# Kernel optimization log

Measured on AMD Instinct MI355X. Metric: run time of the kernel, lower is better.

Reference implementation:

```python
import jax, jax.numpy as jnp
import numpy as np

N_HEAD = 16
D_HEAD = 64
D_MODEL = 1024  # d_qry = d_key = d_val
D_HIDDEN = N_HEAD * D_HEAD


def setup_inputs() -> dict:
    key = jax.random.key(0)
    ks = jax.random.split(key, 9)
    b, n = 2, 2048
    s = 0.02
    return {
        "qry": jax.random.normal(ks[0], (b, n, D_MODEL), jnp.float32),
        "key": jax.random.normal(ks[1], (b, n, D_MODEL), jnp.float32),
        "val": jax.random.normal(ks[2], (b, n, D_MODEL), jnp.float32),
        "mask": jax.random.randint(ks[3], (b, n), 0, 2) > 0,  # key-side padding mask
        "Wq": jax.random.normal(ks[4], (D_MODEL, D_HIDDEN), jnp.float32) * s,
        "Wk": jax.random.normal(ks[5], (D_MODEL, D_HIDDEN), jnp.float32) * s,
        "Wv": jax.random.normal(ks[6], (D_MODEL, D_HIDDEN), jnp.float32) * s,
        "Wo": jax.random.normal(ks[7], (D_HIDDEN, D_MODEL), jnp.float32) * s,
        "bo": jax.random.normal(ks[8], (D_MODEL,), jnp.float32) * s,
    }


def reference(qry, key, val, mask, Wq, Wk, Wv, Wo, bo):
    b, n, _ = qry.shape
    scale = D_HEAD ** 0.5
    # projections, split into heads: [b, h, n, d]
    q = (qry @ Wq).reshape(b, n, N_HEAD, D_HEAD).transpose(0, 2, 1, 3)
    k = (key @ Wk).reshape(b, n, N_HEAD, D_HEAD).transpose(0, 2, 1, 3)
    v = (val @ Wv).reshape(b, n, N_HEAD, D_HEAD).transpose(0, 2, 1, 3)
    sim = jnp.einsum('bhid,bhjd->bhij', q, k) / scale  # full O(n^2) scores
    # key-side padding mask broadcast over heads and query positions
    sim = jnp.where(mask[:, None, None, :], sim, jnp.float32(-1e32))
    attn = jax.nn.softmax(sim, axis=-1)
    # NOTE: original applies dropout to `sim` after computing attn (a no-op on
    # the output); dropout=0.0 regardless, so attention weights are `attn`.
    x = jnp.einsum('bhij,bhjd->bhid', attn, v)
    x = x.transpose(0, 2, 1, 3).reshape(b, n, D_HIDDEN)
    return x @ Wo + bo
```

## Files before the change

kernel.cpp:

```cpp
#include <hip/hip_runtime.h>
#include <hip/hip_bf16.h>

using u16 = unsigned short;
using u32 = unsigned int;
using short8 = __attribute__((ext_vector_type(8))) short;
using f32x4  = __attribute__((ext_vector_type(4))) float;
using u32x4  = __attribute__((ext_vector_type(4))) u32;
using u32x2  = __attribute__((ext_vector_type(2))) u32;

union V16 { u32x4 u; short8 s; };

__device__ __forceinline__ u16 f2b(float f) {
  u32 u = __float_as_uint(f);
  u32 r = (u + 0x7FFFu + ((u >> 16) & 1u)) >> 16;
  return (u16)r;
}
__device__ __forceinline__ u32 pk2(u16 a, u16 b) {
  return (u32)a | ((u32)b << 16);
}
__device__ __forceinline__ u32 cvtpk(float lo, float hi) {
  u32 r;
  asm("v_cvt_pk_bf16_f32 %0, %1, %2" : "=v"(r) : "v"(lo), "v"(hi));
  return r;
}
__device__ __forceinline__ float ex2(float x) {
  float r;
  asm("v_exp_f32 %0, %1" : "=v"(r) : "v"(x));
  return r;
}
__device__ __forceinline__ void gld16(const u16* g, u16* l) {
  __builtin_amdgcn_global_load_lds(
      (const __attribute__((address_space(1))) u32*)g,
      (__attribute__((address_space(3))) u32*)l, 16, 0, 0);
}

#define KSCALE 0.18033688011f
#define SMAX   12.0f


__global__ __launch_bounds__(256) void wconv(
    const float* __restrict__ Wq, const float* __restrict__ Wk,
    const float* __restrict__ Wv, const float* __restrict__ Wo,
    u16* __restrict__ Wt, u16* __restrict__ WoT)
{
  __shared__ u16 T[64][130];
  const int zz = blockIdx.z;
  const float* src = (zz == 0) ? Wq : (zz == 1) ? Wk : (zz == 2) ? Wv : Wo;
  u16* dst = (zz < 3) ? (Wt + (size_t)zz * 1048576) : WoT;
  const int nt = blockIdx.x, ks = blockIdx.y;
  const int tid = threadIdx.x;

  {
    const int kl = tid >> 2, nl0 = (tid & 3) * 32;
    const float* sp = src + (size_t)(ks * 64 + kl) * 1024 + nt * 128 + nl0;
#pragma unroll
    for (int i = 0; i < 8; ++i) {
      f32x4 x = *(const f32x4*)(sp + i * 4);
      T[kl][nl0 + i * 4 + 0] = f2b(x[0]);
      T[kl][nl0 + i * 4 + 1] = f2b(x[1]);
      T[kl][nl0 + i * 4 + 2] = f2b(x[2]);
      T[kl][nl0 + i * 4 + 3] = f2b(x[3]);
    }
  }
  __syncthreads();

  const int c = tid >> 4, l0 = (tid & 15) * 4;
  u16* dp = dst + ((size_t)(nt * 16 + ks) * 16 + c) * 512 + l0 * 8;
#pragma unroll
  for (int dl = 0; dl < 4; ++dl) {
    const int l = l0 + dl;
    const int kl = (c & 1) * 32 + (l >> 4) * 8;
    const int nl = (c >> 3) * 64 + ((c >> 1) & 3) * 16 + (l & 15);
    u32x4 u;
#pragma unroll
    for (int p = 0; p < 4; ++p)
      u[p] = pk2(T[kl + 2 * p][nl], T[kl + 2 * p + 1][nl]);
    *(u32x4*)(dp + dl * 8) = u;
  }
}

__global__ __launch_bounds__(256) void aconv(
    const float* __restrict__ Aq, const float* __restrict__ Ak,
    const float* __restrict__ Av, u16* __restrict__ Af,
    int z0, size_t zstride)
{
  const int z = blockIdx.z + z0;
  const float* A = (z == 0) ? Aq : (z == 1) ? Ak : Av;
  u16* dst = Af + (size_t)blockIdx.z * zstride;
  const int ks = blockIdx.x, mt = blockIdx.y;
  const int tid = threadIdx.x;
  const int r = tid >> 1, h = tid & 1;

  const f32x4* sp = (const f32x4*)(A + (size_t)(mt * 128 + r) * 1024 + ks * 64 + h * 32);
  const int c = ((r >> 6) << 3) | (((r >> 4) & 3) << 1) | h;
  u16* dp = dst + ((size_t)(mt * 16 + ks) * 16 + c) * 512 + (r & 15) * 8;

#pragma unroll
  for (int lg = 0; lg < 4; ++lg) {
    f32x4 x0 = sp[2 * lg], x1 = sp[2 * lg + 1];
    u32x4 u;
    u[0] = cvtpk(x0[0], x0[1]); u[1] = cvtpk(x0[2], x0[3]);
    u[2] = cvtpk(x1[0], x1[1]); u[3] = cvtpk(x1[2], x1[3]);
    *(u32x4*)(dp + lg * 128) = u;
  }
}

__global__ __launch_bounds__(256) void maskscan(
    const int* __restrict__ mask, int* __restrict__ cidx,
    float* __restrict__ cbias, int* __restrict__ ntb,
    u16* __restrict__ Kimg, u16* __restrict__ Vimg)
{
  const int h = blockIdx.x, b = blockIdx.y;
  const int tid = threadIdx.x;
  __shared__ int ssum[256];

  int m8[8], s = 0;
#pragma unroll
  for (int i = 0; i < 8; ++i) {
    m8[i] = mask[b * 2048 + tid * 8 + i] ? 1 : 0;
    s += m8[i];
  }
  ssum[tid] = s;
  __syncthreads();
  for (int off = 1; off < 256; off <<= 1) {
    int v = (tid >= off) ? ssum[tid - off] : 0;
    __syncthreads();
    ssum[tid] += v;
    __syncthreads();
  }
  const int nvalid = ssum[255];
  int run = ssum[tid] - s;

  if (h == 0) {
#pragma unroll
    for (int i = 0; i < 8; ++i) {
      cidx[b * 2048 + tid * 8 + i] = m8[i] ? run : -1;
      run += m8[i];
    }
#pragma unroll
    for (int i = 0; i < 8; ++i) {
      const int idx = tid * 8 + i;
      cbias[b * 2048 + idx] = (idx < nvalid) ? -SMAX : -1e30f;
    }
    if (tid == 0) ntb[b] = (nvalid + 63) >> 6;
  }

  const int pend = ((nvalid + 63) >> 6) << 6;
  for (int p = nvalid + tid; p < pend; p += 256) {
    const int kt2 = p >> 6, r = p & 63;
    const size_t base = ((size_t)((b * 16 + h) * 32 + kt2)) * 4096;
    const int t2 = ((r >> 5) << 1) | ((r >> 2) & 1);
    const int ll2 = (((r >> 3) & 3) << 2) | (r & 3);
#pragma unroll
    for (int s2 = 0; s2 < 2; ++s2)
#pragma unroll
      for (int lgk = 0; lgk < 4; ++lgk)
#pragma unroll
        for (int e = 0; e < 8; ++e)
          Kimg[base + (t2 * 2 + s2) * 512 + (lgk * 16 + ll2) * 8 + e] = 0;
    const int sv = r >> 5, lgv = (r >> 3) & 3, e0 = r & 7;
#pragma unroll
    for (int td = 0; td < 4; ++td)
#pragma unroll
      for (int llv = 0; llv < 16; ++llv)
        Vimg[base + (sv * 4 + td) * 512 + (lgv * 16 + llv) * 8 + e0] = 0;
  }
}

__global__ __launch_bounds__(512, 4) void gemm_qkv_k(
    const u16* __restrict__ Af, const u16* __restrict__ Wt,
    u16* __restrict__ Qw, u16* __restrict__ Kw, u16* __restrict__ Vw,
    const int* __restrict__ cidx, int z0, size_t azs)
{
  __shared__ u16 As[2][8192];
  __shared__ u16 Bs[2][8192];

  const int L = blockIdx.x;
  const int xcd = L & 7, idx = L >> 3;
  const int mt = (xcd << 2) | (idx & 3);
  const int nt = (idx >> 2) & 7;
  const int zi = idx >> 5;
  const int z = z0 + zi;

  const u16* Aimg = Af + (size_t)zi * azs;
  const u16* Bimg = Wt + (size_t)z * 1048576;
  u16* O = (z == 0) ? Qw : (z == 1) ? Kw : Vw;

  const int tid = threadIdx.x;
  const int w = tid >> 6, l = tid & 63, lg = l >> 4, ll = l & 15;
  const int wr = w >> 2, wc = w & 3;
  const size_t ab = (size_t)mt * 131072;
  const size_t bb = (size_t)nt * 131072;

  f32x4 acc[4][2];
#pragma unroll
  for (int i = 0; i < 4; ++i)
#pragma unroll
    for (int t = 0; t < 2; ++t)
      acc[i][t] = (f32x4){0.f, 0.f, 0.f, 0.f};

#define QKV_ISSUE(ksx, buf) do {                                           \
    const size_t ao_ = ab + (size_t)(ksx) * 8192;                          \
    const size_t bo_ = bb + (size_t)(ksx) * 8192;                          \
    gld16(Aimg + ao_ + (size_t)w * 512 + l * 8,       &As[buf][w * 512]);  \
    gld16(Aimg + ao_ + (size_t)(w + 8) * 512 + l * 8, &As[buf][(w + 8) * 512]); \
    gld16(Bimg + bo_ + (size_t)w * 512 + l * 8,       &Bs[buf][w * 512]);  \
    gld16(Bimg + bo_ + (size_t)(w + 8) * 512 + l * 8, &Bs[buf][(w + 8) * 512]); \
  } while (0)

  QKV_ISSUE(0, 0);

  for (int ks = 0; ks < 16; ++ks) {
    const int cur = ks & 1;
    asm volatile("s_waitcnt vmcnt(0)" ::: "memory");
    __builtin_amdgcn_sched_barrier(0);
    __builtin_amdgcn_s_barrier();
    __builtin_amdgcn_sched_barrier(0);

    if (ks + 1 < 16) QKV_ISSUE(ks + 1, cur ^ 1);

    short8 afr[2][4], bfr[2][2];
#pragma unroll
    for (int kk = 0; kk < 2; ++kk) {
#pragma unroll
      for (int i = 0; i < 4; ++i) {
        V16 v; v.u = *(const u32x4*)&As[cur][(wr * 8 + i * 2 + kk) * 512 + l * 8];
        afr[kk][i] = v.s;
      }
#pragma unroll
      for (int t = 0; t < 2; ++t) {
        V16 v; v.u = *(const u32x4*)&Bs[cur][((wc >> 1) * 8 + ((wc & 1) * 2 + t) * 2 + kk) * 512 + l * 8];
        bfr[kk][t] = v.s;
      }
    }
#pragma unroll
    for (int kk = 0; kk < 2; ++kk)
#pragma unroll
      for (int i = 0; i < 4; ++i)
#pragma unroll
        for (int t = 0; t < 2; ++t)
          acc[i][t] = __builtin_amdgcn_mfma_f32_16x16x32_bf16(afr[kk][i], bfr[kk][t], acc[i][t], 0, 0, 0);
  }
#undef QKV_ISSUE

  const int m0 = mt * 128, n0 = nt * 128;
  if (z == 0) {
#pragma unroll
    for (int i = 0; i < 4; ++i)
#pragma unroll
      for (int t = 0; t < 2; ++t) {
        const int n = n0 + wc * 32 + t * 16 + ll;
        const int h = n >> 6, dd = n & 63;
#pragma unroll
        for (int j = 0; j < 4; ++j) {
          const int m = m0 + wr * 64 + i * 16 + lg * 4 + j;
          const int bbk = m >> 11, pos = m & 2047;
          O[((size_t)(bbk * 16 + h) * 2048 + pos) * 64 + dd] = f2b(acc[i][t][j]);
        }
      }
  } else if (z == 1) {
#pragma unroll
    for (int i = 0; i < 4; ++i)
#pragma unroll
      for (int t = 0; t < 2; ++t) {
        const int n = n0 + wc * 32 + t * 16 + ll;
        const int h = n >> 6, dd = n & 63;
        const int s = dd >> 5, lgk = (dd >> 3) & 3, e = dd & 7;
        const int m_ = m0 + wr * 64 + i * 16 + lg * 4;
        const int bbk = m_ >> 11, pos0 = m_ & 2047;
        const int4 cp = *(const int4*)&cidx[bbk * 2048 + pos0];
        const int cpa[4] = {cp.x, cp.y, cp.z, cp.w};
#pragma unroll
        for (int j = 0; j < 4; ++j) {
          const int pp = cpa[j];
          if (pp >= 0) {
            const int kt2 = pp >> 6, r = pp & 63;
            const int t2 = ((r >> 5) << 1) | ((r >> 2) & 1);
            const int ll2 = (((r >> 3) & 3) << 2) | (r & 3);
            O[((size_t)((bbk * 16 + h) * 32 + kt2)) * 4096 + (t2 * 2 + s) * 512 + (lgk * 16 + ll2) * 8 + e]
                = f2b(acc[i][t][j] * KSCALE);
          }
        }
      }
  } else {
#pragma unroll
    for (int i = 0; i < 4; ++i)
#pragma unroll
      for (int t = 0; t < 2; ++t) {
        const int n = n0 + wc * 32 + t * 16 + ll;
        const int h = n >> 6, dd = n & 63;
        const int td = dd >> 4, llv = dd & 15;
        const int m_ = m0 + wr * 64 + i * 16 + lg * 4;
        const int bbk = m_ >> 11, pos0 = m_ & 2047;
        const int4 cp = *(const int4*)&cidx[bbk * 2048 + pos0];
        const int cpa[4] = {cp.x, cp.y, cp.z, cp.w};
#pragma unroll
        for (int j = 0; j < 4; ++j) {
          const int pp = cpa[j];
          if (pp >= 0) {
            const int kt2 = pp >> 6, kk = pp & 63;
            const int s = kk >> 5, lgv = (kk >> 3) & 3, e0 = kk & 7;
            O[((size_t)((bbk * 16 + h) * 32 + kt2)) * 4096 + (s * 4 + td) * 512 + (lgv * 16 + llv) * 8 + e0]
                = f2b(acc[i][t][j]);
          }
        }
      }
  }
}

__global__ __launch_bounds__(256) void attn_k(
    const u16* __restrict__ Q, const u16* __restrict__ Kt, const u16* __restrict__ Vt,
    const float* __restrict__ cbias, const int* __restrict__ ntb,
    u16* __restrict__ Xf)
{
  __shared__ u16 Ls[2][8192];

  const int tid = threadIdx.x;
  const int w = tid >> 6, l = tid & 63, lg = l >> 4, ll = l & 15;
  const int qb = blockIdx.x, h = blockIdx.y, b = blockIdx.z;
  const size_t qbase = (size_t)(b * 16 + h) * 2048 * 64;
  const size_t tbase = (size_t)((b * 16 + h) * 32) * 4096;
  const int q0 = qb * 128 + w * 32;
  const int ntiles = ntb[b];

  short8 aq[2][2];
#pragma unroll
  for (int g = 0; g < 2; ++g)
#pragma unroll
    for (int s = 0; s < 2; ++s) {
      V16 v; v.u = *(const u32x4*)&Q[qbase + (size_t)(q0 + g * 16 + ll) * 64 + s * 32 + lg * 8];
      aq[g][s] = v.s;
    }

  float lrow[2] = {0.f, 0.f};
  f32x4 o[2][4];
#pragma unroll
  for (int g = 0; g < 2; ++g)
#pragma unroll
    for (int td = 0; td < 4; ++td) o[g][td] = (f32x4){0.f, 0.f, 0.f, 0.f};

  u32x4 rg[4];
#pragma unroll
  for (int q = 0; q < 4; ++q) {
    const int c = w * 4 + q;
    const u16* src = (c < 8) ? Kt : Vt;
    rg[q] = *(const u32x4*)&src[tbase + (c & 7) * 512 + l * 8];
  }
#pragma unroll
  for (int q = 0; q < 4; ++q)
    *(u32x4*)&Ls[0][(w * 4 + q) * 512 + l * 8] = rg[q];
  if (ntiles > 1) {
#pragma unroll
    for (int q = 0; q < 4; ++q) {
      const int c = w * 4 + q;
      const u16* src = (c < 8) ? Kt : Vt;
      rg[q] = *(const u32x4*)&src[tbase + 4096 + (c & 7) * 512 + l * 8];
    }
  }
  asm volatile("s_waitcnt lgkmcnt(0)" ::: "memory");
  __builtin_amdgcn_sched_barrier(0);
  __builtin_amdgcn_s_barrier();
  __builtin_amdgcn_sched_barrier(0);

  for (int kt = 0; kt < ntiles; ++kt) {
    const int cur = kt & 1;
    const int j0 = kt * 64;
    const u16* Lc = Ls[cur];

    f32x4 sc[2][4];
    __builtin_amdgcn_s_setprio(1);
#pragma unroll
    for (int t = 0; t < 4; ++t) {
      short8 bk0, bk1;
      { V16 v; v.u = *(const u32x4*)&Lc[(t * 2 + 0) * 512 + l * 8]; bk0 = v.s; }
      { V16 v; v.u = *(const u32x4*)&Lc[(t * 2 + 1) * 512 + l * 8]; bk1 = v.s; }
      f32x4 a0 = (f32x4){0.f, 0.f, 0.f, 0.f};
      f32x4 a1 = (f32x4){0.f, 0.f, 0.f, 0.f};
      a0 = __builtin_amdgcn_mfma_f32_16x16x32_bf16(bk0, aq[0][0], a0, 0, 0, 0);
      a1 = __builtin_amdgcn_mfma_f32_16x16x32_bf16(bk0, aq[1][0], a1, 0, 0, 0);
      a0 = __builtin_amdgcn_mfma_f32_16x16x32_bf16(bk1, aq[0][1], a0, 0, 0, 0);
      a1 = __builtin_amdgcn_mfma_f32_16x16x32_bf16(bk1, aq[1][1], a1, 0, 0, 0);
      const f32x4 cb = *(const f32x4*)&cbias[b * 2048 + j0 + ((t >> 1) << 5) + ((t & 1) << 2) + (lg << 3)];
#pragma unroll
      for (int j = 0; j < 4; ++j) {
        sc[0][t][j] = a0[j] + cb[j];
        sc[1][t][j] = a1[j] + cb[j];
      }
    }
    __builtin_amdgcn_s_setprio(0);

#pragma unroll
    for (int g = 0; g < 2; ++g) {
      f32x4 s4 = (f32x4){0.f, 0.f, 0.f, 0.f};
#pragma unroll
      for (int t = 0; t < 4; ++t)
#pragma unroll
        for (int j = 0; j < 4; ++j) {
          sc[g][t][j] = ex2(sc[g][t][j]);
          s4[j] += sc[g][t][j];
        }
      float rs = (s4[0] + s4[1]) + (s4[2] + s4[3]);
      rs += __shfl_xor(rs, 16);
      rs += __shfl_xor(rs, 32);
      lrow[g] += rs;
    }

    __builtin_amdgcn_s_setprio(1);
#pragma unroll
    for (int s = 0; s < 2; ++s) {
      V16 pb0, pb1;
      pb0.u[0] = cvtpk(sc[0][2 * s][0], sc[0][2 * s][1]);
      pb0.u[1] = cvtpk(sc[0][2 * s][2], sc[0][2 * s][3]);
      pb0.u[2] = cvtpk(sc[0][2 * s + 1][0], sc[0][2 * s + 1][1]);
      pb0.u[3] = cvtpk(sc[0][2 * s + 1][2], sc[0][2 * s + 1][3]);
      pb1.u[0] = cvtpk(sc[1][2 * s][0], sc[1][2 * s][1]);
      pb1.u[1] = cvtpk(sc[1][2 * s][2], sc[1][2 * s][3]);
      pb1.u[2] = cvtpk(sc[1][2 * s + 1][0], sc[1][2 * s + 1][1]);
      pb1.u[3] = cvtpk(sc[1][2 * s + 1][2], sc[1][2 * s + 1][3]);
#pragma unroll
      for (int td = 0; td < 4; ++td) {
        V16 v; v.u = *(const u32x4*)&Lc[4096 + (s * 4 + td) * 512 + l * 8];
        o[0][td] = __builtin_amdgcn_mfma_f32_16x16x32_bf16(v.s, pb0.s, o[0][td], 0, 0, 0);
        o[1][td] = __builtin_amdgcn_mfma_f32_16x16x32_bf16(v.s, pb1.s, o[1][td], 0, 0, 0);
      }
    }
    __builtin_amdgcn_s_setprio(0);

    if (kt + 1 < ntiles) {
#pragma unroll
      for (int q = 0; q < 4; ++q)
        *(u32x4*)&Ls[cur ^ 1][(w * 4 + q) * 512 + l * 8] = rg[q];
    }
    if (kt + 2 < ntiles) {
#pragma unroll
      for (int q = 0; q < 4; ++q) {
        const int c = w * 4 + q;
        const u16* src = (c < 8) ? Kt : Vt;
        rg[q] = *(const u32x4*)&src[tbase + (size_t)(kt + 2) * 4096 + (c & 7) * 512 + l * 8];
      }
    }
    asm volatile("s_waitcnt lgkmcnt(0)" ::: "memory");
    __builtin_amdgcn_sched_barrier(0);
    __builtin_amdgcn_s_barrier();
    __builtin_amdgcn_sched_barrier(0);
  }

#pragma unroll
  for (int g = 0; g < 2; ++g) {
    const float inv = 1.f / lrow[g];
    const int m = b * 2048 + q0 + g * 16 + ll;
    const int mt = m >> 7, mr = m & 127;
    const int e0 = (lg & 1) * 4;
#pragma unroll
    for (int td = 0; td < 4; ++td) {
      const int c = ((mr >> 6) << 3) | (((mr >> 4) & 3) << 1) | (td >> 1);
      const int lA = (((td << 1) + (lg >> 1)) & 3) * 16 + (mr & 15);
      u32x2 wv;
      wv[0] = cvtpk(o[g][td][0] * inv, o[g][td][1] * inv);
      wv[1] = cvtpk(o[g][td][2] * inv, o[g][td][3] * inv);
      *(u32x2*)&Xf[((size_t)(mt * 16 + h) * 16 + c) * 512 + lA * 8 + e0] = wv;
    }
  }
}

__global__ __launch_bounds__(512, 4) void gemm_out_k(
    const u16* __restrict__ Xf, const u16* __restrict__ WoF,
    const float* __restrict__ bo, float* __restrict__ out)
{
  __shared__ u16 As[2][8192];
  __shared__ u16 Bs[2][8192];

  const int L = blockIdx.x;
  const int xcd = L & 7, idx = L >> 3;
  const int mt = (xcd << 2) | (idx & 3);
  const int nt = idx >> 2;

  const int tid = threadIdx.x;
  const int w = tid >> 6, l = tid & 63, lg = l >> 4, ll = l & 15;
  const int wr = w >> 2, wc = w & 3;
  const size_t ab = (size_t)mt * 131072;
  const size_t bb = (size_t)nt * 131072;

  f32x4 acc[4][2];
#pragma unroll
  for (int i = 0; i < 4; ++i)
#pragma unroll
    for (int t = 0; t < 2; ++t)
      acc[i][t] = (f32x4){0.f, 0.f, 0.f, 0.f};

#define OUT_ISSUE(ksx, buf) do {                                           \
    const size_t ao_ = ab + (size_t)(ksx) * 8192;                          \
    const size_t bo_ = bb + (size_t)(ksx) * 8192;                          \
    gld16(Xf + ao_ + (size_t)w * 512 + l * 8,        &As[buf][w * 512]);   \
    gld16(Xf + ao_ + (size_t)(w + 8) * 512 + l * 8,  &As[buf][(w + 8) * 512]); \
    gld16(WoF + bo_ + (size_t)w * 512 + l * 8,       &Bs[buf][w * 512]);   \
    gld16(WoF + bo_ + (size_t)(w + 8) * 512 + l * 8, &Bs[buf][(w + 8) * 512]); \
  } while (0)

  OUT_ISSUE(0, 0);

  for (int ks = 0; ks < 16; ++ks) {
    const int cur = ks & 1;
    asm volatile("s_waitcnt vmcnt(0)" ::: "memory");
    __builtin_amdgcn_sched_barrier(0);
    __builtin_amdgcn_s_barrier();
    __builtin_amdgcn_sched_barrier(0);

    if (ks + 1 < 16) OUT_ISSUE(ks + 1, cur ^ 1);

    short8 afr[2][4], bfr[2][2];
#pragma unroll
    for (int kk = 0; kk < 2; ++kk) {
#pragma unroll
      for (int i = 0; i < 4; ++i) {
        V16 v; v.u = *(const u32x4*)&As[cur][(wr * 8 + i * 2 + kk) * 512 + l * 8];
        afr[kk][i] = v.s;
      }
#pragma unroll
      for (int t = 0; t < 2; ++t) {
        V16 v; v.u = *(const u32x4*)&Bs[cur][((wc >> 1) * 8 + ((wc & 1) * 2 + t) * 2 + kk) * 512 + l * 8];
        bfr[kk][t] = v.s;
      }
    }
#pragma unroll
    for (int kk = 0; kk < 2; ++kk)
#pragma unroll
      for (int i = 0; i < 4; ++i)
#pragma unroll
        for (int t = 0; t < 2; ++t)
          acc[i][t] = __builtin_amdgcn_mfma_f32_16x16x32_bf16(afr[kk][i], bfr[kk][t], acc[i][t], 0, 0, 0);
  }
#undef OUT_ISSUE

  const int m0 = mt * 128, n0 = nt * 128;
#pragma unroll
  for (int i = 0; i < 4; ++i)
#pragma unroll
    for (int t = 0; t < 2; ++t) {
      const int n = n0 + wc * 32 + t * 16 + ll;
      const float bv = bo[n];
#pragma unroll
      for (int j = 0; j < 4; ++j) {
        const int m = m0 + wr * 64 + i * 16 + lg * 4 + j;
        out[(size_t)m * 1024 + n] = acc[i][t][j] + bv;
      }
    }
}

extern "C" void kernel_launch(void* const* d_in, const int* in_sizes, int n_in,
                              void* d_out, int out_size, void* d_ws, size_t ws_size,
                              hipStream_t stream) {
  const float* qry = (const float*)d_in[0];
  const float* key = (const float*)d_in[1];
  const float* val = (const float*)d_in[2];
  const int* mask  = (const int*)d_in[3];
  const float* Wq  = (const float*)d_in[4];
  const float* Wk  = (const float*)d_in[5];
  const float* Wv  = (const float*)d_in[6];
  const float* Wo  = (const float*)d_in[7];
  const float* bo  = (const float*)d_in[8];
  float* out = (float*)d_out;

  char* ws = (char*)d_ws;
  u16* Wt  = (u16*)(ws);
  u16* WoT = (u16*)(ws + 6291456);
  u16* Qw  = (u16*)(ws + 8388608);
  u16* Kw  = (u16*)(ws + 16777216);
  u16* Vw  = (u16*)(ws + 25165824);
  u16* Af  = (u16*)(ws + 33554432);
  u16* Xw  = (u16*)(ws + 33554432);

  int*   cidx  = (int*)d_out;
  float* cbias = (float*)((char*)d_out + 16384);
  int*   ntb   = (int*)((char*)d_out + 32768);

  wconv<<<dim3(8, 16, 4), 256, 0, stream>>>(Wq, Wk, Wv, Wo, Wt, WoT);
  maskscan<<<dim3(16, 2), 256, 0, stream>>>(mask, cidx, cbias, ntb, Kw, Vw);

  const bool big = (ws_size >= 58720256ull);
  if (big) {
    aconv<<<dim3(16, 32, 3), 256, 0, stream>>>(qry, key, val, Af, 0, 4194304);
    gemm_qkv_k<<<dim3(768, 1, 1), 512, 0, stream>>>(Af, Wt, Qw, Kw, Vw, cidx, 0, 4194304);
  } else {
    for (int z = 0; z < 3; ++z) {
      aconv<<<dim3(16, 32, 1), 256, 0, stream>>>(qry, key, val, Af, z, 0);
      gemm_qkv_k<<<dim3(256, 1, 1), 512, 0, stream>>>(Af, Wt, Qw, Kw, Vw, cidx, z, 0);
    }
  }
  attn_k<<<dim3(16, 16, 2), 256, 0, stream>>>(Qw, Kw, Vw, cbias, ntb, Xw);
  gemm_out_k<<<dim3(256, 1, 1), 512, 0, stream>>>(Xw, WoT, bo, out);
}
```

Measured before the change: 112.5 us.

## Widen QKV GEMM tile to 128x256 with triple-buffered half-K stages

```diff
diff --git a/kernel.cpp b/kernel.cpp
--- a/kernel.cpp
+++ b/kernel.cpp
@@ -172,84 +172,93 @@
     u16* __restrict__ Qw, u16* __restrict__ Kw, u16* __restrict__ Vw,
     const int* __restrict__ cidx, int z0, size_t azs)
 {
-  __shared__ u16 As[2][8192];
-  __shared__ u16 Bs[2][8192];
+  __shared__ u16 As[3][4096];
+  __shared__ u16 Bs[3][8192];
 
   const int L = blockIdx.x;
   const int xcd = L & 7, idx = L >> 3;
-  const int mt = (xcd << 2) | (idx & 3);
-  const int nt = (idx >> 2) & 7;
-  const int zi = idx >> 5;
-  const int z = z0 + zi;
+  const int mt  = (xcd << 2) | (idx & 3);
+  const int ntB = (idx >> 2) & 3;
+  const int zi  = idx >> 4;
+  const int z   = z0 + zi;
 
   const u16* Aimg = Af + (size_t)zi * azs;
-  const u16* Bimg = Wt + (size_t)z * 1048576;
+  const u16* B0 = Wt + (size_t)z * 1048576 + (size_t)(2 * ntB) * 131072;
+  const u16* B1 = B0 + 131072;
   u16* O = (z == 0) ? Qw : (z == 1) ? Kw : Vw;
 
   const int tid = threadIdx.x;
   const int w = tid >> 6, l = tid & 63, lg = l >> 4, ll = l & 15;
   const int wr = w >> 2, wc = w & 3;
-  const size_t ab = (size_t)mt * 131072;
-  const size_t bb = (size_t)nt * 131072;
-
-  f32x4 acc[4][2];
+  const size_t abase = (size_t)mt * 131072;
+
+  f32x4 acc[4][4];
 #pragma unroll
   for (int i = 0; i < 4; ++i)
 #pragma unroll
-    for (int t = 0; t < 2; ++t)
+    for (int t = 0; t < 4; ++t)
       acc[i][t] = (f32x4){0.f, 0.f, 0.f, 0.f};
 
-#define QKV_ISSUE(ksx, buf) do {                                           \
-    const size_t ao_ = ab + (size_t)(ksx) * 8192;                          \
-    const size_t bo_ = bb + (size_t)(ksx) * 8192;                          \
-    gld16(Aimg + ao_ + (size_t)w * 512 + l * 8,       &As[buf][w * 512]);  \
-    gld16(Aimg + ao_ + (size_t)(w + 8) * 512 + l * 8, &As[buf][(w + 8) * 512]); \
-    gld16(Bimg + bo_ + (size_t)w * 512 + l * 8,       &Bs[buf][w * 512]);  \
-    gld16(Bimg + bo_ + (size_t)(w + 8) * 512 + l * 8, &Bs[buf][(w + 8) * 512]); \
+#define QKV_ISSUE(sx, bf) do {                                              \
+    const int ksi_ = (sx) >> 1, kkx_ = (sx) & 1;                            \
+    const size_t ao_ = abase + (size_t)ksi_ * 8192;                         \
+    const size_t bo_ = (size_t)ksi_ * 8192;                                 \
+    _Pragma("unroll")                                                       \
+    for (int q = 0; q < 3; ++q) {                                           \
+      const int cc = w * 3 + q;                                             \
+      if (cc < 8) {                                                         \
+        const int o_ = cc >> 2, f_ = cc & 3;                                \
+        gld16(Aimg + ao_ + (o_ * 8 + f_ * 2 + kkx_) * 512 + l * 8,          \
+              &As[bf][(o_ * 4 + f_) * 512]);                                \
+      } else {                                                              \
+        const int j_ = cc - 8;                                              \
+        const int hb_ = j_ >> 3, o_ = (j_ >> 2) & 1, f_ = j_ & 3;           \
+        const u16* bsrc_ = hb_ ? B1 : B0;                                   \
+        gld16(bsrc_ + bo_ + (o_ * 8 + f_ * 2 + kkx_) * 512 + l * 8,         \
+              &Bs[bf][(hb_ * 8 + o_ * 4 + f_) * 512]);                      \
+      }                                                                     \
+    }                                                                       \
   } while (0)
 
   QKV_ISSUE(0, 0);
-
-  for (int ks = 0; ks < 16; ++ks) {
-    const int cur = ks & 1;
-    asm volatile("s_waitcnt vmcnt(0)" ::: "memory");
+  QKV_ISSUE(1, 1);
+
+  for (int s = 0; s < 32; ++s) {
+    const int cur = s % 3;
+    if (s < 31) asm volatile("s_waitcnt vmcnt(3)" ::: "memory");
+    else        asm volatile("s_waitcnt vmcnt(0)" ::: "memory");
     __builtin_amdgcn_sched_barrier(0);
     __builtin_amdgcn_s_barrier();
     __builtin_amdgcn_sched_barrier(0);
 
-    if (ks + 1 < 16) QKV_ISSUE(ks + 1, cur ^ 1);
-
-    short8 afr[2][4], bfr[2][2];
-#pragma unroll
-    for (int kk = 0; kk < 2; ++kk) {
-#pragma unroll
-      for (int i = 0; i < 4; ++i) {
-        V16 v; v.u = *(const u32x4*)&As[cur][(wr * 8 + i * 2 + kk) * 512 + l * 8];
-        afr[kk][i] = v.s;
-      }
-#pragma unroll
-      for (int t = 0; t < 2; ++t) {
-        V16 v; v.u = *(const u32x4*)&Bs[cur][((wc >> 1) * 8 + ((wc & 1) * 2 + t) * 2 + kk) * 512 + l * 8];
-        bfr[kk][t] = v.s;
-      }
-    }
-#pragma unroll
-    for (int kk = 0; kk < 2; ++kk)
-#pragma unroll
-      for (int i = 0; i < 4; ++i)
-#pragma unroll
-        for (int t = 0; t < 2; ++t)
-          acc[i][t] = __builtin_amdgcn_mfma_f32_16x16x32_bf16(afr[kk][i], bfr[kk][t], acc[i][t], 0, 0, 0);
+    if (s + 2 < 32) QKV_ISSUE(s + 2, (s + 2) % 3);
+
+    short8 afr[4], bfr[4];
+#pragma unroll
+    for (int i = 0; i < 4; ++i) {
+      V16 v; v.u = *(const u32x4*)&As[cur][(wr * 4 + i) * 512 + l * 8];
+      afr[i] = v.s;
+    }
+#pragma unroll
+    for (int t = 0; t < 4; ++t) {
+      V16 v; v.u = *(const u32x4*)&Bs[cur][((wc >> 1) * 8 + (wc & 1) * 4 + t) * 512 + l * 8];
+      bfr[t] = v.s;
+    }
+#pragma unroll
+    for (int i = 0; i < 4; ++i)
+#pragma unroll
+      for (int t = 0; t < 4; ++t)
+        acc[i][t] = __builtin_amdgcn_mfma_f32_16x16x32_bf16(afr[i], bfr[t], acc[i][t], 0, 0, 0);
   }
 #undef QKV_ISSUE
 
-  const int m0 = mt * 128, n0 = nt * 128;
+  const int m0 = mt * 128, n0 = ntB * 256;
   if (z == 0) {
 #pragma unroll
     for (int i = 0; i < 4; ++i)
 #pragma unroll
-      for (int t = 0; t < 2; ++t) {
-        const int n = n0 + wc * 32 + t * 16 + ll;
+      for (int t = 0; t < 4; ++t) {
+        const int n = n0 + wc * 64 + t * 16 + ll;
         const int h = n >> 6, dd = n & 63;
 #pragma unroll
         for (int j = 0; j < 4; ++j) {
@@ -262,8 +271,8 @@
 #pragma unroll
     for (int i = 0; i < 4; ++i)
 #pragma unroll
-      for (int t = 0; t < 2; ++t) {
-        const int n = n0 + wc * 32 + t * 16 + ll;
+      for (int t = 0; t < 4; ++t) {
+        const int n = n0 + wc * 64 + t * 16 + ll;
         const int h = n >> 6, dd = n & 63;
         const int s = dd >> 5, lgk = (dd >> 3) & 3, e = dd & 7;
         const int m_ = m0 + wr * 64 + i * 16 + lg * 4;
@@ -286,8 +295,8 @@
 #pragma unroll
     for (int i = 0; i < 4; ++i)
 #pragma unroll
-      for (int t = 0; t < 2; ++t) {
-        const int n = n0 + wc * 32 + t * 16 + ll;
+      for (int t = 0; t < 4; ++t) {
+        const int n = n0 + wc * 64 + t * 16 + ll;
         const int h = n >> 6, dd = n & 63;
         const int td = dd >> 4, llv = dd & 15;
         const int m_ = m0 + wr * 64 + i * 16 + lg * 4;
@@ -580,11 +589,11 @@
   const bool big = (ws_size >= 58720256ull);
   if (big) {
     aconv<<<dim3(16, 32, 3), 256, 0, stream>>>(qry, key, val, Af, 0, 4194304);
-    gemm_qkv_k<<<dim3(768, 1, 1), 512, 0, stream>>>(Af, Wt, Qw, Kw, Vw, cidx, 0, 4194304);
+    gemm_qkv_k<<<dim3(384, 1, 1), 512, 0, stream>>>(Af, Wt, Qw, Kw, Vw, cidx, 0, 4194304);
   } else {
     for (int z = 0; z < 3; ++z) {
       aconv<<<dim3(16, 32, 1), 256, 0, stream>>>(qry, key, val, Af, z, 0);
-      gemm_qkv_k<<<dim3(256, 1, 1), 512, 0, stream>>>(Af, Wt, Qw, Kw, Vw, cidx, z, 0);
+      gemm_qkv_k<<<dim3(128, 1, 1), 512, 0, stream>>>(Af, Wt, Qw, Kw, Vw, cidx, z, 0);
     }
   }
   attn_k<<<dim3(16, 16, 2), 256, 0, stream>>>(Qw, Kw, Vw, cbias, ntb, Xw);
```

Result: no change. 112.7 us (+0.2%).
